# Kernel tuning notes

Measured on AMD Instinct MI355X. Metric: run time of the kernel, lower is better.

## Reference

```python
import jax, jax.numpy as jnp
import numpy as np

B, N, C, H, D = 1, 256, 128, 4, 32  # batch, seq, c_z, no_heads, c_hidden
INF = 1e9
LN_EPS = 1e-5


def setup_inputs() -> dict:
    key = jax.random.key(0)
    ks = jax.random.split(key, 8)
    s = 0.02
    return {
        "x": jax.random.normal(ks[0], (B, N, N, C), jnp.float32),
        "mask": jnp.ones((B, N, N), jnp.float32),
        "ln_w": jnp.ones((C,), jnp.float32),
        "ln_b": jnp.zeros((C,), jnp.float32),
        "w_bias": jax.random.normal(ks[1], (H, C), jnp.float32) * s,  # tri-bias linear (no bias)
        "wq": jax.random.normal(ks[2], (C, H, D), jnp.float32) * s,
        "wk": jax.random.normal(ks[3], (C, H, D), jnp.float32) * s,
        "wv": jax.random.normal(ks[4], (C, H, D), jnp.float32) * s,
        "wg": jax.random.normal(ks[5], (C, H, D), jnp.float32) * s,
        "bg": jnp.ones((H * D,), jnp.float32),  # gating bias init = 1 (OpenFold)
        "wo": jax.random.normal(ks[6], (C, H * D), jnp.float32) * s,
        "bo": jnp.zeros((C,), jnp.float32),
    }


def reference(x, mask, ln_w, ln_b, w_bias, wq, wk, wv, wg, bg, wo, bo):
    scale = 1.0 / np.sqrt(D)
    # Ending-node: transpose the two N dims, then operate like starting node
    x_t = jnp.swapaxes(x, 1, 2)          # [B, J, I, C] -> treat as [B, N, N, C]
    m_t = jnp.swapaxes(mask, 1, 2)       # [B, N, N]
    # layer norm over channels
    mu = jnp.mean(x_t, axis=-1, keepdims=True)
    var = jnp.var(x_t, axis=-1, keepdims=True)
    xn = (x_t - mu) * jax.lax.rsqrt(var + LN_EPS) * ln_w + ln_b
    # mask bias: inf * (mask - 1), broadcast over heads and query dim
    mask_bias = INF * (m_t[:, :, None, None, :] - 1.0)     # [B, N, 1, 1, N]
    # triangle bias: linear -> permute_final_dims (2,0,1) -> unsqueeze(-4)
    tri_bias = jnp.einsum("bijc,hc->bhij", xn, w_bias)[:, None]  # [B, 1, H, N, N]
    # gated MHA over the last sequence axis
    q = jnp.einsum("bijc,chd->bijhd", xn, wq) * scale
    k = jnp.einsum("bijc,chd->bijhd", xn, wk)
    v = jnp.einsum("bijc,chd->bijhd", xn, wv)
    a = jnp.einsum("bijhd,bikhd->bihjk", q, k) + mask_bias + tri_bias  # [B,N,H,N,N]
    a = jax.nn.softmax(a, axis=-1)
    o = jnp.einsum("bihjk,bikhd->bijhd", a, v)                        # [B,N,N,H,D]
    g = jax.nn.sigmoid(jnp.einsum("bijc,chd->bijhd", xn, wg) + bg.reshape(H, D))
    o = (o * g).reshape(B, N, N, H * D)
    out = jnp.einsum("bijk,ok->bijo", o, wo) + bo                     # [B,N,N,C]
    return jnp.swapaxes(out, 1, 2)
```

## Files before the change

kernel.cpp:

```cpp
#include <hip/hip_runtime.h>

#define N 256
#define C 128
#define H 4
#define D 32
#define LN_EPS 1e-5f
#define INFB 1e9f
#define SCALE 0.17677669529663687f

typedef __bf16 bf16x8 __attribute__((ext_vector_type(8)));
typedef __bf16 bf16x2 __attribute__((ext_vector_type(2)));
typedef _Float16 halfx8 __attribute__((ext_vector_type(8)));
typedef float floatx4 __attribute__((ext_vector_type(4)));

__device__ __forceinline__ floatx4 mfma16(bf16x8 a, bf16x8 b, floatx4 c) {
    return __builtin_amdgcn_mfma_f32_16x16x32_bf16(a, b, c, 0, 0, 0);
}
__device__ __forceinline__ floatx4 mfma16h(halfx8 a, halfx8 b, floatx4 c) {
    return __builtin_amdgcn_mfma_f32_16x16x32_f16(a, b, c, 0, 0, 0);
}

__global__ __launch_bounds__(256) void wt_kernel(
    const float* __restrict__ wq, const float* __restrict__ wk,
    const float* __restrict__ wv, const float* __restrict__ wg,
    const float* __restrict__ wo, __bf16* __restrict__ wTg,
    _Float16* __restrict__ woh)
{
    const int mat = blockIdx.x >> 3, seg = blockIdx.x & 7;
    if (mat == 4) {
        #pragma unroll
        for (int rep = 0; rep < 8; ++rep) {
            const int idx = seg * 2048 + rep * 256 + threadIdx.x;
            woh[idx] = (_Float16)wo[idx];
        }
        return;
    }
    const float* __restrict__ ws_ = (mat == 0) ? wq : (mat == 1) ? wk
                                  : (mat == 2) ? wv : wg;
    #pragma unroll
    for (int rep = 0; rep < 8; ++rep) {
        const int idx = seg * 2048 + rep * 256 + threadIdx.x;
        const int n = idx >> 7, c = idx & 127;
        wTg[mat * 16384 + n * 128 + c] = (__bf16)ws_[c * 128 + n];
    }
}

__global__ __launch_bounds__(256) void ln_kernel(
    const float* __restrict__ x, const float* __restrict__ lnw,
    const float* __restrict__ lnb, const float* __restrict__ wbias,
    __bf16* __restrict__ xn, float* __restrict__ tbp)
{
    const int t = threadIdx.x;
    const int wv = t >> 6, lane = t & 63;
    const int r = blockIdx.x * 4 + wv;
    const int a = r >> 8, b = r & 255;

    const float2 v = *(const float2*)&x[((size_t)b * N + a) * C + lane * 2];
    float s  = v.x + v.y;
    float ss = v.x * v.x + v.y * v.y;
    #pragma unroll
    for (int o = 32; o; o >>= 1) {
        s  += __shfl_xor(s,  o);
        ss += __shfl_xor(ss, o);
    }
    const float mu  = s * (1.0f / 128.0f);
    const float var = ss * (1.0f / 128.0f) - mu * mu;
    const float rs  = rsqrtf(var + LN_EPS);

    const float2 lw = *(const float2*)&lnw[lane * 2];
    const float2 lb = *(const float2*)&lnb[lane * 2];
    const float y0 = (v.x - mu) * rs * lw.x + lb.x;
    const float y1 = (v.y - mu) * rs * lw.y + lb.y;

    bf16x2 xo; xo[0] = (__bf16)y0; xo[1] = (__bf16)y1;
    *(bf16x2*)&xn[(size_t)r * C + lane * 2] = xo;

    const int jb   = a >> 4;
    const int lnA  = (b & 15) | (((a & 15) >> 2) << 4);
    const int slot = ((b >> 4) << 2) | (a & 3);
    #pragma unroll
    for (int hh = 0; hh < H; ++hh) {
        const float2 wb2 = *(const float2*)&wbias[hh * C + lane * 2];
        float tv = y0 * wb2.x + y1 * wb2.y;
        #pragma unroll
        for (int o = 32; o; o >>= 1) tv += __shfl_xor(tv, o);
        if (lane == 0)
            tbp[(size_t)(((hh * 16 + jb) * 64 + lnA) * 64 + slot)] = tv;
    }
}

__global__ __launch_bounds__(256, 3) void proj_kernel(
    const __bf16* __restrict__ xn, const __bf16* __restrict__ wTg,
    __bf16* __restrict__ qbuf, __bf16* __restrict__ kbuf,
    __bf16* __restrict__ vbuf, __bf16* __restrict__ gbuf)
{
    __shared__ __bf16 Cs[4][64 * 72];

    const int mat = blockIdx.y;
    const int t = threadIdx.x, w = t >> 6, lane = t & 63;
    const int ln16 = lane & 15, quad = lane >> 4;
    const int wr = w >> 1, wc = w & 1;
    const int m_base = blockIdx.x * 128 + wr * 64;
    const int n_base = wc * 64;
    const __bf16* __restrict__ wT = wTg + mat * 16384;

    floatx4 Cf[4][4];
    const floatx4 z4 = {0.f, 0.f, 0.f, 0.f};
    #pragma unroll
    for (int mt = 0; mt < 4; ++mt)
        #pragma unroll
        for (int nt = 0; nt < 4; ++nt) Cf[mt][nt] = z4;

    #pragma unroll
    for (int ks = 0; ks < 4; ++ks) {
        bf16x8 Af[4], Bf[4];
        #pragma unroll
        for (int mt = 0; mt < 4; ++mt)
            Af[mt] = *(const bf16x8*)&xn[(size_t)(m_base + mt*16 + ln16) * 128 + ks*32 + quad*8];
        #pragma unroll
        for (int nt = 0; nt < 4; ++nt)
            Bf[nt] = *(const bf16x8*)&wT[(n_base + nt*16 + ln16) * 128 + ks*32 + quad*8];
        #pragma unroll
        for (int mt = 0; mt < 4; ++mt)
            #pragma unroll
            for (int nt = 0; nt < 4; ++nt)
                Cf[mt][nt] = mfma16(Af[mt], Bf[nt], Cf[mt][nt]);
    }

    const float scl = (mat == 0) ? SCALE : 1.0f;
    __bf16* __restrict__ Cw = &Cs[w][0];
    #pragma unroll
    for (int mt = 0; mt < 4; ++mt)
        #pragma unroll
        for (int nt = 0; nt < 4; ++nt)
            #pragma unroll
            for (int r = 0; r < 4; ++r)
                Cw[(mt*16 + quad*4 + r) * 72 + nt*16 + ln16] =
                    (__bf16)(Cf[mt][nt][r] * scl);

    __bf16* __restrict__ dst = (mat == 0) ? qbuf : (mat == 1) ? kbuf
                             : (mat == 2) ? vbuf : gbuf;
    const int m = m_base + lane;
    const int i = m >> 8, jk = m & 255;
    #pragma unroll
    for (int hf = 0; hf < 2; ++hf) {
        const int hh = wc * 2 + hf;
        __bf16* __restrict__ drow = dst + (((size_t)i*4 + hh)*256 + jk)*32;
        #pragma unroll
        for (int u = 0; u < 4; ++u)
            *(bf16x8*)&drow[u*8] = *(const bf16x8*)&Cw[lane*72 + hf*32 + u*8];
    }
}

__global__ __launch_bounds__(256, 2) void attn_kernel(
    const float* __restrict__ tbp, const float* __restrict__ mask,
    const float* __restrict__ bg,
    const __bf16* __restrict__ qbuf, const __bf16* __restrict__ kbuf,
    const __bf16* __restrict__ vbuf, const __bf16* __restrict__ gbuf,
    _Float16* __restrict__ ogh)
{
    const int bid = blockIdx.x;
    const int i = bid & 255, h = bid >> 8;
    const int t = threadIdx.x, w = t >> 6, lane = t & 63;
    const int ln16 = lane & 15, quad = lane >> 4;

    __shared__ __align__(16) __bf16 Ks[256 * 40];
    __shared__ __align__(16) __bf16 VT[32 * 264];
    __shared__ __align__(16) __bf16 Pw[4][16 * 264];
    __shared__ float mb[256];

    const size_t hb = (size_t)i * 4 + h;
    const __bf16* __restrict__ qb = qbuf + hb * 8192;
    const __bf16* __restrict__ kb = kbuf + hb * 8192;
    const __bf16* __restrict__ vb = vbuf + hb * 8192;
    const __bf16* __restrict__ gb = gbuf + hb * 8192;

    #pragma unroll
    for (int u = 0; u < 4; ++u)
        *(bf16x8*)&Ks[t * 40 + u * 8] = *(const bf16x8*)&kb[t * 32 + u * 8];
    #pragma unroll
    for (int u = 0; u < 4; ++u) {
        const bf16x8 vv = *(const bf16x8*)&vb[t * 32 + u * 8];
        #pragma unroll
        for (int e = 0; e < 8; ++e) VT[(u*8 + e) * 264 + t] = vv[e];
    }
    mb[t] = INFB * (mask[(size_t)t * N + i] - 1.0f);
    __syncthreads();

    const float bg0 = bg[h*32 + ln16], bg1 = bg[h*32 + 16 + ln16];

    float mbv[16];
    #pragma unroll
    for (int kt = 0; kt < 16; ++kt) mbv[kt] = mb[kt*16 + ln16];

    __bf16* __restrict__ Pww = &Pw[w][0];
    const floatx4 z4 = {0.f, 0.f, 0.f, 0.f};
    _Float16* __restrict__ ogb = ogh + ((size_t)h * 256 + i) * 8192;

    #pragma unroll 1
    for (int jt = 0; jt < 4; ++jt) {
        const int jrow0 = w*64 + jt*16;
        const float* __restrict__ tbl =
            tbp + ((size_t)((h*16 + (w*4 + jt))*64 + lane) << 6);
        const bf16x8 Qf = *(const bf16x8*)&qb[(jrow0 + ln16)*32 + quad*8];

        floatx4 S[16];
        #pragma unroll
        for (int kt = 0; kt < 16; ++kt) {
            const bf16x8 Kf = *(const bf16x8*)&Ks[(kt*16 + ln16)*40 + quad*8];
            S[kt] = mfma16(Qf, Kf, z4);
        }

        #pragma unroll
        for (int kt = 0; kt < 16; ++kt) {
            const float4 tb4 = *(const float4*)&tbl[kt*4];
            const float mbk = mbv[kt];
            S[kt][0] += mbk + tb4.x;
            S[kt][1] += mbk + tb4.y;
            S[kt][2] += mbk + tb4.z;
            S[kt][3] += mbk + tb4.w;
        }

        float mrow[4], l[4];
        #pragma unroll
        for (int r = 0; r < 4; ++r) {
            float mx = S[0][r];
            #pragma unroll
            for (int kt = 1; kt < 16; ++kt) mx = fmaxf(mx, S[kt][r]);
            #pragma unroll
            for (int off = 1; off < 16; off <<= 1) mx = fmaxf(mx, __shfl_xor(mx, off));
            mrow[r] = mx; l[r] = 0.f;
        }
        #pragma unroll
        for (int kt = 0; kt < 16; ++kt)
            #pragma unroll
            for (int r = 0; r < 4; ++r) {
                const float p = __expf(S[kt][r] - mrow[r]);
                S[kt][r] = p; l[r] += p;
            }
        #pragma unroll
        for (int r = 0; r < 4; ++r)
            #pragma unroll
            for (int off = 1; off < 16; off <<= 1) l[r] += __shfl_xor(l[r], off);

        #pragma unroll
        for (int kt = 0; kt < 16; ++kt)
            #pragma unroll
            for (int r = 0; r < 4; ++r)
                Pww[(quad*4 + r)*264 + kt*16 + ln16] = (__bf16)S[kt][r];

        floatx4 O0 = z4, O1 = z4;
        #pragma unroll
        for (int ks = 0; ks < 8; ++ks) {
            const bf16x8 Af = *(const bf16x8*)&Pww[ln16*264 + ks*32 + quad*8];
            const bf16x8 V0 = *(const bf16x8*)&VT[ln16*264 + ks*32 + quad*8];
            const bf16x8 V1 = *(const bf16x8*)&VT[(16 + ln16)*264 + ks*32 + quad*8];
            O0 = mfma16(Af, V0, O0);
            O1 = mfma16(Af, V1, O1);
        }

        _Float16* Po = (_Float16*)Pww;
        #pragma unroll
        for (int r = 0; r < 4; ++r) {
            const float inv = 1.0f / l[r];
            const int jrow = jrow0 + quad*4 + r;
            const float g0 = (float)gb[jrow*32 + ln16];
            const float g1 = (float)gb[jrow*32 + 16 + ln16];
            const float gate0 = 1.0f / (1.0f + __expf(-(g0 + bg0)));
            const float gate1 = 1.0f / (1.0f + __expf(-(g1 + bg1)));
            Po[(quad*4 + r)*264 + ln16]      = (_Float16)(O0[r] * inv * gate0);
            Po[(quad*4 + r)*264 + 16 + ln16] = (_Float16)(O1[r] * inv * gate1);
        }
        {
            const int rr = lane >> 2, cc = lane & 3;
            const halfx8 ov = *(const halfx8*)&Po[rr*264 + cc*8];
            *(halfx8*)&ogb[(size_t)(jrow0 + rr)*32 + cc*8] = ov;
        }
    }
}

__global__ __launch_bounds__(256, 4) void outproj_kernel(
    const _Float16* __restrict__ og, const _Float16* __restrict__ woh,
    const float* __restrict__ bo, float* __restrict__ out)
{
    const int t = threadIdx.x, w = t >> 6, lane = t & 63;
    const int ln16 = lane & 15, quad = lane >> 4;
    const int wr = w >> 1, wc = w & 1;
    const int m_base = blockIdx.x * 128 + wr * 64;
    const int n_base = wc * 64;

    floatx4 Cf[4][4];
    const floatx4 z4 = {0.f, 0.f, 0.f, 0.f};
    #pragma unroll
    for (int mt = 0; mt < 4; ++mt)
        #pragma unroll
        for (int nt = 0; nt < 4; ++nt) Cf[mt][nt] = z4;

    #pragma unroll
    for (int ks = 0; ks < 4; ++ks) {
        halfx8 Af[4], Bf[4];
        #pragma unroll
        for (int mt = 0; mt < 4; ++mt)
            Af[mt] = *(const halfx8*)&og[(size_t)ks*2097152 + (size_t)(m_base + mt*16 + ln16)*32 + quad*8];
        #pragma unroll
        for (int nt = 0; nt < 4; ++nt)
            Bf[nt] = *(const halfx8*)&woh[(n_base + nt*16 + ln16)*128 + ks*32 + quad*8];
        #pragma unroll
        for (int mt = 0; mt < 4; ++mt)
            #pragma unroll
            for (int nt = 0; nt < 4; ++nt)
                Cf[mt][nt] = mfma16h(Af[mt], Bf[nt], Cf[mt][nt]);
    }

    float bov[4];
    #pragma unroll
    for (int nt = 0; nt < 4; ++nt) bov[nt] = bo[n_base + nt*16 + ln16];

    #pragma unroll
    for (int mt = 0; mt < 4; ++mt)
        #pragma unroll
        for (int r = 0; r < 4; ++r) {
            const int m = m_base + mt*16 + quad*4 + r;
            const size_t orow = (size_t)(m & 255) * 256 + (m >> 8);
            #pragma unroll
            for (int nt = 0; nt < 4; ++nt)
                out[orow*128 + n_base + nt*16 + ln16] = Cf[mt][nt][r] + bov[nt];
        }
}

extern "C" void kernel_launch(void* const* d_in, const int* in_sizes, int n_in,
                              void* d_out, int out_size, void* d_ws, size_t ws_size,
                              hipStream_t stream) {
    const float* x     = (const float*)d_in[0];
    const float* mask  = (const float*)d_in[1];
    const float* lnw   = (const float*)d_in[2];
    const float* lnb   = (const float*)d_in[3];
    const float* wbias = (const float*)d_in[4];
    const float* wq    = (const float*)d_in[5];
    const float* wk    = (const float*)d_in[6];
    const float* wv    = (const float*)d_in[7];
    const float* wg    = (const float*)d_in[8];
    const float* bg    = (const float*)d_in[9];
    const float* wo    = (const float*)d_in[10];
    const float* bo    = (const float*)d_in[11];
    float* out = (float*)d_out;

    char* wsb = (char*)d_ws;
    __bf16*    xn   = (__bf16*)   (wsb);
    float*     tbp  = (float*)    (wsb + 16777216);
    __bf16*    wTg  = (__bf16*)   (wsb + 17825792);
    _Float16*  woh  = (_Float16*) (wsb + 17956864);
    __bf16*    qbuf = (__bf16*)   (wsb + 17989632);
    __bf16*    kbuf = (__bf16*)   (wsb + 34766848);
    __bf16*    vbuf = (__bf16*)   (wsb + 51544064);
    __bf16*    gbuf = (__bf16*)   (wsb + 68321280);
    _Float16*  ogh  = (_Float16*) (wsb + 85098496);

    wt_kernel<<<40, 256, 0, stream>>>(wq, wk, wv, wg, wo, wTg, woh);
    ln_kernel<<<16384, 256, 0, stream>>>(x, lnw, lnb, wbias, xn, tbp);
    proj_kernel<<<dim3(512, 4), 256, 0, stream>>>(xn, wTg, qbuf, kbuf, vbuf, gbuf);
    attn_kernel<<<1024, 256, 0, stream>>>(tbp, mask, bg, qbuf, kbuf, vbuf, gbuf, ogh);
    outproj_kernel<<<512, 256, 0, stream>>>(ogh, woh, bo, out);
}
```

Baseline: 251.4 us.

## Transpose QK^T tiles and pass softmax probabilities to PV via lane shuffles

Result: slower. 355.9 us (+41.6%).

```diff
diff --git a/kernel.cpp b/kernel.cpp
--- a/kernel.cpp
+++ b/kernel.cpp
@@ -11,6 +11,7 @@
 typedef __bf16 bf16x8 __attribute__((ext_vector_type(8)));
 typedef __bf16 bf16x2 __attribute__((ext_vector_type(2)));
 typedef _Float16 halfx8 __attribute__((ext_vector_type(8)));
+typedef _Float16 halfx4 __attribute__((ext_vector_type(4)));
 typedef float floatx4 __attribute__((ext_vector_type(4)));
 
 __device__ __forceinline__ floatx4 mfma16(bf16x8 a, bf16x8 b, floatx4 c) {
@@ -76,8 +77,8 @@
     *(bf16x2*)&xn[(size_t)r * C + lane * 2] = xo;
 
     const int jb   = a >> 4;
-    const int lnA  = (b & 15) | (((a & 15) >> 2) << 4);
-    const int slot = ((b >> 4) << 2) | (a & 3);
+    const int lnA  = (a & 15) | (((b & 15) >> 2) << 4);
+    const int slot = ((b >> 4) << 2) | (b & 3);
     #pragma unroll
     for (int hh = 0; hh < H; ++hh) {
         const float2 wb2 = *(const float2*)&wbias[hh * C + lane * 2];
@@ -152,7 +153,7 @@
     }
 }
 
-__global__ __launch_bounds__(256, 2) void attn_kernel(
+__global__ __launch_bounds__(256, 3) void attn_kernel(
     const float* __restrict__ tbp, const float* __restrict__ mask,
     const float* __restrict__ bg,
     const __bf16* __restrict__ qbuf, const __bf16* __restrict__ kbuf,
@@ -166,7 +167,7 @@
 
     __shared__ __align__(16) __bf16 Ks[256 * 40];
     __shared__ __align__(16) __bf16 VT[32 * 264];
-    __shared__ __align__(16) __bf16 Pw[4][16 * 264];
+    __shared__ __align__(16) _Float16 Pe[4][16 * 44];
     __shared__ float mb[256];
 
     const size_t hb = (size_t)i * 4 + h;
@@ -189,13 +190,12 @@
 
     const float bg0 = bg[h*32 + ln16], bg1 = bg[h*32 + 16 + ln16];
 
-    float mbv[16];
-    #pragma unroll
-    for (int kt = 0; kt < 16; ++kt) mbv[kt] = mb[kt*16 + ln16];
-
-    __bf16* __restrict__ Pww = &Pw[w][0];
+    _Float16* __restrict__ Pww = &Pe[w][0];
     const floatx4 z4 = {0.f, 0.f, 0.f, 0.f};
     _Float16* __restrict__ ogb = ogh + ((size_t)h * 256 + i) * 8192;
+
+    const int idxA = ln16 + ((quad & 1) << 5);
+    const int idxB = idxA + 16;
 
     #pragma unroll 1
     for (int jt = 0; jt < 4; ++jt) {
@@ -208,72 +208,105 @@
         #pragma unroll
         for (int kt = 0; kt < 16; ++kt) {
             const bf16x8 Kf = *(const bf16x8*)&Ks[(kt*16 + ln16)*40 + quad*8];
-            S[kt] = mfma16(Qf, Kf, z4);
+            S[kt] = mfma16(Kf, Qf, z4);
         }
 
         #pragma unroll
         for (int kt = 0; kt < 16; ++kt) {
             const float4 tb4 = *(const float4*)&tbl[kt*4];
-            const float mbk = mbv[kt];
-            S[kt][0] += mbk + tb4.x;
-            S[kt][1] += mbk + tb4.y;
-            S[kt][2] += mbk + tb4.z;
-            S[kt][3] += mbk + tb4.w;
-        }
-
-        float mrow[4], l[4];
-        #pragma unroll
-        for (int r = 0; r < 4; ++r) {
-            float mx = S[0][r];
-            #pragma unroll
-            for (int kt = 1; kt < 16; ++kt) mx = fmaxf(mx, S[kt][r]);
-            #pragma unroll
-            for (int off = 1; off < 16; off <<= 1) mx = fmaxf(mx, __shfl_xor(mx, off));
-            mrow[r] = mx; l[r] = 0.f;
-        }
+            const float4 mb4 = *(const float4*)&mb[kt*16 + quad*4];
+            S[kt][0] += mb4.x + tb4.x;
+            S[kt][1] += mb4.y + tb4.y;
+            S[kt][2] += mb4.z + tb4.z;
+            S[kt][3] += mb4.w + tb4.w;
+        }
+
+        floatx4 a0 = S[0], a1 = S[1], a2 = S[2], a3 = S[3];
+        #pragma unroll
+        for (int kt = 4; kt < 16; kt += 4) {
+            #pragma unroll
+            for (int e = 0; e < 4; ++e) {
+                a0[e] = fmaxf(a0[e], S[kt+0][e]);
+                a1[e] = fmaxf(a1[e], S[kt+1][e]);
+                a2[e] = fmaxf(a2[e], S[kt+2][e]);
+                a3[e] = fmaxf(a3[e], S[kt+3][e]);
+            }
+        }
+        float mx;
+        {
+            floatx4 m01, m23;
+            #pragma unroll
+            for (int e = 0; e < 4; ++e) { m01[e] = fmaxf(a0[e], a1[e]); m23[e] = fmaxf(a2[e], a3[e]); }
+            mx = fmaxf(fmaxf(fmaxf(m01[0], m01[1]), fmaxf(m01[2], m01[3])),
+                       fmaxf(fmaxf(m23[0], m23[1]), fmaxf(m23[2], m23[3])));
+        }
+        mx = fmaxf(mx, __shfl_xor(mx, 16));
+        mx = fmaxf(mx, __shfl_xor(mx, 32));
+
+        floatx4 lacc = z4;
         #pragma unroll
         for (int kt = 0; kt < 16; ++kt)
             #pragma unroll
-            for (int r = 0; r < 4; ++r) {
-                const float p = __expf(S[kt][r] - mrow[r]);
-                S[kt][r] = p; l[r] += p;
+            for (int e = 0; e < 4; ++e) {
+                const float p = __expf(S[kt][e] - mx);
+                S[kt][e] = p; lacc[e] += p;
             }
-        #pragma unroll
-        for (int r = 0; r < 4; ++r)
-            #pragma unroll
-            for (int off = 1; off < 16; off <<= 1) l[r] += __shfl_xor(l[r], off);
-
-        #pragma unroll
-        for (int kt = 0; kt < 16; ++kt)
-            #pragma unroll
-            for (int r = 0; r < 4; ++r)
-                Pww[(quad*4 + r)*264 + kt*16 + ln16] = (__bf16)S[kt][r];
+        float l = (lacc[0] + lacc[1]) + (lacc[2] + lacc[3]);
+        l += __shfl_xor(l, 16);
+        l += __shfl_xor(l, 32);
+
+        unsigned int U0[16], U1[16];
+        #pragma unroll
+        for (int kt = 0; kt < 16; ++kt) {
+            bf16x2 p0, p1;
+            p0[0] = (__bf16)S[kt][0]; p0[1] = (__bf16)S[kt][1];
+            p1[0] = (__bf16)S[kt][2]; p1[1] = (__bf16)S[kt][3];
+            U0[kt] = __builtin_bit_cast(unsigned int, p0);
+            U1[kt] = __builtin_bit_cast(unsigned int, p1);
+        }
 
         floatx4 O0 = z4, O1 = z4;
         #pragma unroll
         for (int ks = 0; ks < 8; ++ks) {
-            const bf16x8 Af = *(const bf16x8*)&Pww[ln16*264 + ks*32 + quad*8];
+            const unsigned int e0a = __shfl(U0[2*ks],   idxA);
+            const unsigned int f0a = __shfl(U0[2*ks+1], idxA);
+            const unsigned int e1a = __shfl(U1[2*ks],   idxA);
+            const unsigned int f1a = __shfl(U1[2*ks+1], idxA);
+            const unsigned int e0b = __shfl(U0[2*ks],   idxB);
+            const unsigned int f0b = __shfl(U0[2*ks+1], idxB);
+            const unsigned int e1b = __shfl(U1[2*ks],   idxB);
+            const unsigned int f1b = __shfl(U1[2*ks+1], idxB);
+            uint4 pw;
+            pw.x = (quad < 2) ? e0a : f0a;
+            pw.y = (quad < 2) ? e1a : f1a;
+            pw.z = (quad < 2) ? e0b : f0b;
+            pw.w = (quad < 2) ? e1b : f1b;
+            const bf16x8 PA = __builtin_bit_cast(bf16x8, pw);
             const bf16x8 V0 = *(const bf16x8*)&VT[ln16*264 + ks*32 + quad*8];
             const bf16x8 V1 = *(const bf16x8*)&VT[(16 + ln16)*264 + ks*32 + quad*8];
-            O0 = mfma16(Af, V0, O0);
-            O1 = mfma16(Af, V1, O1);
-        }
-
-        _Float16* Po = (_Float16*)Pww;
+            O0 = mfma16(PA, V0, O0);
+            O1 = mfma16(PA, V1, O1);
+        }
+
+        const float invl = 1.0f / l;
         #pragma unroll
         for (int r = 0; r < 4; ++r) {
-            const float inv = 1.0f / l[r];
+            const float inv = __shfl(invl, quad*4 + r);
             const int jrow = jrow0 + quad*4 + r;
             const float g0 = (float)gb[jrow*32 + ln16];
             const float g1 = (float)gb[jrow*32 + 16 + ln16];
             const float gate0 = 1.0f / (1.0f + __expf(-(g0 + bg0)));
             const float gate1 = 1.0f / (1.0f + __expf(-(g1 + bg1)));
-            Po[(quad*4 + r)*264 + ln16]      = (_Float16)(O0[r] * inv * gate0);
-            Po[(quad*4 + r)*264 + 16 + ln16] = (_Float16)(O1[r] * inv * gate1);
+            Pww[(quad*4 + r)*44 + ln16]      = (_Float16)(O0[r] * inv * gate0);
+            Pww[(quad*4 + r)*44 + 16 + ln16] = (_Float16)(O1[r] * inv * gate1);
         }
         {
             const int rr = lane >> 2, cc = lane & 3;
-            const halfx8 ov = *(const halfx8*)&Po[rr*264 + cc*8];
+            const halfx4 lo = *(const halfx4*)&Pww[rr*44 + cc*8];
+            const halfx4 hi = *(const halfx4*)&Pww[rr*44 + cc*8 + 4];
+            halfx8 ov;
+            #pragma unroll
+            for (int e = 0; e < 4; ++e) { ov[e] = lo[e]; ov[4+e] = hi[e]; }
             *(halfx8*)&ogb[(size_t)(jrow0 + rr)*32 + cc*8] = ov;
         }
     }
```
